# Performance work log

Measured on AMD Instinct MI355X. Metric: run time of the kernel, lower is better.

The kernel has to match this reference:

```python
import jax, jax.numpy as jnp
import numpy as np

ZERO = 1e-8
L = 2            # num_gnn_layers
D = 256          # dim_node_features
B = 32           # graphs per batch
NPG = 256        # nodes per graph
N = B * NPG      # total nodes
E = 131072       # edges per edge-type
MAX_TOKENS = 256 # MAX_TOKENS_OF_A_POST
UPD = 0.5        # args.updated_weights_for_A


def _make_edges(k):
    k1, k2, k3 = jax.random.split(k, 3)
    g = jax.random.randint(k1, (E,), 0, B) * NPG          # keep edges within a graph
    src = g + jax.random.randint(k2, (E,), 0, NPG)
    dst = g + jax.random.randint(k3, (E,), 0, NPG)
    return jnp.stack([src, dst]).astype(jnp.int64)


def setup_inputs() -> dict:
    key = jax.random.key(0)
    ks = jax.random.split(key, 12)
    x = jax.random.normal(ks[0], (N, D), dtype=jnp.float32)
    ei_e = _make_edges(ks[1]); ew_e = jax.random.uniform(ks[2], (E,), dtype=jnp.float32)
    ei_p = _make_edges(ks[3]); ew_p = jax.random.uniform(ks[4], (E,), dtype=jnp.float32)
    ei_o = _make_edges(ks[5]); ew_o = jax.random.uniform(ks[6], (E,), dtype=jnp.float32)
    entity_mask = jax.random.randint(ks[7], (B, NPG), 0, 2).astype(bool)
    pattern_mask = jax.random.randint(ks[8], (B, NPG), 0, 2).astype(bool)
    s = 1.0 / np.sqrt(D)
    W_gcn = (jax.random.normal(ks[9], (L, 3, D, D), dtype=jnp.float32) * s)
    b_gcn = jnp.zeros((L, 3, D), dtype=jnp.float32)
    T_dyn = (jax.random.normal(ks[10], (L, D, D), dtype=jnp.float32) * s)
    return {
        'x': x,
        'edge_index_entity': ei_e, 'edge_weight_entity': ew_e,
        'edge_index_pattern': ei_p, 'edge_weight_pattern': ew_p,
        'edge_index_others': ei_o, 'edge_weight_others': ew_o,
        'entity_mask': entity_mask, 'pattern_mask': pattern_mask,
        'W_gcn': W_gcn, 'b_gcn': b_gcn, 'T_dyn': T_dyn,
    }


def _normalized_correlation_matrix(H):
    # cosine-similarity correlation matrix, symmetrically degree-normalized
    nrm = jnp.sqrt(jnp.sum(H * H, axis=1))
    A = (H @ H.T) / (nrm[:, None] * nrm[None, :] + ZERO)
    dinv = 1.0 / jnp.sqrt(jnp.abs(jnp.sum(A, axis=1)) + ZERO)
    return dinv[:, None] * A * dinv[None, :]


def _gcn(H, W, b, ei, ew):
    # GCNConv(add_self_loops=False, normalize=False): scatter-sum of weighted source messages
    msg = (H @ W)[ei[0]] * ew[:, None]                     # [E, D]
    return jax.ops.segment_sum(msg, ei[1], num_segments=N) + b


def _forward(x, we0, wp0, wo0, W_gcn, b_gcn, T_dyn,
             ei_e, ei_p, ei_o, entity_mask, pattern_mask):
    H = x
    A = _normalized_correlation_matrix(H)                  # [N, N]
    for i in range(L):
        if i == 0:
            we, wp, wo = we0, wp0, wo0
        else:
            # diag(one_hot(src) @ A @ one_hot(dst).T) == A[src, dst]
            we = A[ei_e[0], ei_e[1]]
            wp = A[ei_p[0], ei_p[1]]
            wo = A[ei_o[0], ei_o[1]]
        He = _gcn(H, W_gcn[i, 0], b_gcn[i, 0], ei_e, we)
        Hp = _gcn(H, W_gcn[i, 1], b_gcn[i, 1], ei_p, wp)
        Ho = _gcn(H, W_gcn[i, 2], b_gcn[i, 2], ei_o, wo)
        H = jax.nn.relu(He + Hp + Ho)
        A_hat = jax.nn.sigmoid((H @ T_dyn[i]) @ H.T)
        A = (1.0 - UPD) * A + UPD * A_hat
    # per-graph diagonal blocks of A  -> [B, NPG, NPG]
    A4 = A.reshape(B, NPG, B, NPG)
    idx = jnp.arange(B)
    blocks = A4[idx, :, idx, :]
    A_sum = jnp.sum(blocks, axis=-1)                       # [B, NPG]
    ent_cols = jnp.einsum('bij,bj->bi', blocks, entity_mask.astype(A.dtype))
    pat_cols = jnp.einsum('bij,bj->bi', blocks, pattern_mask.astype(A.dtype))
    map_pattern = A_sum - ent_cols
    map_entity = A_sum - pat_cols

    def finish(m):
        mn = jnp.min(m, axis=1, keepdims=True)
        mx = jnp.max(m, axis=1, keepdims=True)
        m = (m - mn) / (mx - mn + ZERO)
        m = m / (jnp.sum(m, axis=1, keepdims=True) + ZERO)
        return m[:, :MAX_TOKENS]                           # padding() with NPG==MAX_TOKENS

    return finish(map_entity), finish(map_pattern)


def reference(x, edge_index_entity, edge_weight_entity,
              edge_index_pattern, edge_weight_pattern,
              edge_index_others, edge_weight_others,
              entity_mask, pattern_mask, W_gcn, b_gcn, T_dyn):
    return _forward(x, edge_weight_entity, edge_weight_pattern, edge_weight_others,
                    W_gcn, b_gcn, T_dyn,
                    edge_index_entity, edge_index_pattern, edge_index_others,
                    entity_mask, pattern_mask)
```

## Files before the change

kernel.cpp:

```cpp
#include <hip/hip_runtime.h>

#define NND   8192
#define DDIM  256
#define NGRP  32
#define ZEROF 1e-8f
#define LSTR  40
#define TSTR  72
#define OFF_AH 0
#define OFF_AL 2560
#define OFF_BH 5120
#define OFF_BL 10240
#define OFF_TT 5120
#define LDS_U16 15360

typedef unsigned short u16;
typedef unsigned long long u64;
typedef __attribute__((ext_vector_type(8))) short short8v;
typedef __attribute__((ext_vector_type(4))) float float4v;

__device__ inline u16 f2bf(float x) {
  unsigned u = __float_as_uint(x);
  u += 0x7fffu + ((u >> 16) & 1u);
  return (u16)(u >> 16);
}
__device__ inline float bf2f(u16 h) { return __uint_as_float((unsigned)h << 16); }
__device__ inline void split2(float x, u16& h, u16& l) {
  h = f2bf(x);
  l = f2bf(x - bf2f(h));
}

__device__ inline float wave_sum(float v) {
#pragma unroll
  for (int off = 32; off > 0; off >>= 1) v += __shfl_down(v, off, 64);
  return v;
}

#define LOAD_REGS(tt, kk)                                                                   \
  {                                                                                         \
    int m_ = tid >> 2, kq_ = (tid & 3) * 8;                                                 \
    size_t aoff_;                                                                           \
    if (MODE == 1)                                                                          \
      aoff_ = (size_t)((tt) * 256 + bym * 64 + m_) * 8192 + (size_t)(g * 256 + (kk) + kq_); \
    else if (MODE == 2 || MODE == 3)                                                        \
      aoff_ = (size_t)(g * 256 + bym * 64 + m_) * 256 + (kk) + kq_;                         \
    else                                                                                    \
      aoff_ = (size_t)(bym * 64 + m_) * 256 + (kk) + kq_;                                   \
    rAh = *(const short8v*)&Ah_g[aoff_];                                                    \
    rAl = *(const short8v*)&Al_g[aoff_];                                                    \
    if (MODE == 1) {                                                                        \
      int n_ = tid >> 2, kq2_ = (tid & 3) * 8;                                              \
      size_t cb_ = (((size_t)g * 3 + (tt)) << 16) + (size_t)(col0 + n_) * 256 + (kk) + kq2_;\
      const float* pb_ = Bfp + (QW ? cb_ * 2 : cb_);                                        \
      rBf[0] = *(const float4*)pb_;                                                         \
      rBf[1] = *(const float4*)(pb_ + 4);                                                   \
      if (QW) {                                                                             \
        rBf[2] = *(const float4*)(pb_ + 8);                                                 \
        rBf[3] = *(const float4*)(pb_ + 12);                                                \
      }                                                                                     \
    } else if (HALF) {                                                                      \
      int n_ = tid & 63, kq2_ = (tid >> 6) * 8;                                             \
      size_t boff_ = (size_t)(((MODE == 2 || MODE == 3) ? g * 256 : 0) + col0 + n_) * 256   \
                     + (kk) + kq2_;                                                         \
      rBh0 = *(const short8v*)&Bh_g[boff_];                                                 \
      rBl0 = *(const short8v*)&Bl_g[boff_];                                                 \
    } else {                                                                                \
      int n_ = tid & 127, kq2_ = (tid >> 7) * 16;                                           \
      size_t boff_ = (size_t)(col0 + n_) * 256 + (kk) + kq2_;                               \
      rBh0 = *(const short8v*)&Bh_g[boff_]; rBh1 = *(const short8v*)&Bh_g[boff_ + 8];       \
      rBl0 = *(const short8v*)&Bl_g[boff_]; rBl1 = *(const short8v*)&Bl_g[boff_ + 8];       \
    }                                                                                       \
  }

template<int MODE, bool HALF, bool QW = false>
__device__ __forceinline__ void mfma_body(
    u16* lds,
    const u16* __restrict__ Ah_g, const u16* __restrict__ Al_g,
    const u16* __restrict__ Bh_g, const u16* __restrict__ Bl_g,
    const float* __restrict__ Bfp,
    float* __restrict__ Cf, u16* __restrict__ Ch, u16* __restrict__ Cl,
    const float* __restrict__ nrm, const float* __restrict__ dinv,
    const float* __restrict__ bias,
    int bxm, int bym, int g) {
  u16* Ahs = lds + OFF_AH;
  u16* Als = lds + OFF_AL;
  u16* Bhs = lds + OFF_BH;
  u16* Bls = lds + OFF_BL;
  u16* Tt  = lds + OFF_TT;
  const int NJ = HALF ? 2 : 4;
  const int tid = threadIdx.x;
  const int col0 = bxm * (HALF ? 64 : 128);
  const int w = tid >> 6, lane = tid & 63;
  const int lm = lane & 15, lq = lane >> 4;
  const int wr = (w >> 1) * 32, wc = (w & 1) * (HALF ? 32 : 64);

  float4v acc[2][4];
#pragma unroll
  for (int i = 0; i < 2; ++i)
#pragma unroll
    for (int j = 0; j < NJ; ++j) acc[i][j] = (float4v)0.f;

  short8v rAh, rAl, rBh0, rBh1, rBl0, rBl1;
  float4 rBf[4];
  const int TOTAL = (MODE == 1) ? 24 : 8;

  LOAD_REGS(0, 0);
  for (int step = 0; step < TOTAL; ++step) {
    if (step) __syncthreads();
    {
      int m = tid >> 2, kq = (tid & 3) * 8;
      *(short8v*)&Ahs[m * LSTR + kq] = rAh;
      *(short8v*)&Als[m * LSTR + kq] = rAl;
    }
    if (MODE == 1) {
      int n = tid >> 2, kq2 = (tid & 3) * 8;
      float vals[8];
      if (QW) {
        u64 vv[8];
        *(float4*)&vv[0] = rBf[0]; *(float4*)&vv[2] = rBf[1];
        *(float4*)&vv[4] = rBf[2]; *(float4*)&vv[6] = rBf[3];
#pragma unroll
        for (int q = 0; q < 8; ++q)
          vals[q] = (float)(vv[q] & 0xFFFFFFFFFFFFull) * 0x1p-32f;
      } else {
        vals[0] = rBf[0].x; vals[1] = rBf[0].y; vals[2] = rBf[0].z; vals[3] = rBf[0].w;
        vals[4] = rBf[1].x; vals[5] = rBf[1].y; vals[6] = rBf[1].z; vals[7] = rBf[1].w;
      }
      u16 hh[8], ll[8];
#pragma unroll
      for (int q = 0; q < 8; ++q) split2(vals[q], hh[q], ll[q]);
      *(short8v*)&Bhs[n * LSTR + kq2] = *(short8v*)hh;
      *(short8v*)&Bls[n * LSTR + kq2] = *(short8v*)ll;
    } else if (HALF) {
      int n = tid & 63, kq2 = (tid >> 6) * 8;
      *(short8v*)&Bhs[n * LSTR + kq2] = rBh0;
      *(short8v*)&Bls[n * LSTR + kq2] = rBl0;
    } else {
      int n = tid & 127, kq2 = (tid >> 7) * 16;
      *(short8v*)&Bhs[n * LSTR + kq2] = rBh0; *(short8v*)&Bhs[n * LSTR + kq2 + 8] = rBh1;
      *(short8v*)&Bls[n * LSTR + kq2] = rBl0; *(short8v*)&Bls[n * LSTR + kq2 + 8] = rBl1;
    }
    __syncthreads();
    int nxt = step + 1;
    if (nxt < TOTAL) {
      int tt = nxt >> 3, kk = (nxt & 7) * 32;
      LOAD_REGS(tt, kk);
    }
    short8v ah[2], al[2], bh[4], bl[4];
#pragma unroll
    for (int i = 0; i < 2; ++i) {
      int r = wr + i * 16 + lm;
      ah[i] = *(const short8v*)&Ahs[r * LSTR + lq * 8];
      al[i] = *(const short8v*)&Als[r * LSTR + lq * 8];
    }
#pragma unroll
    for (int j = 0; j < NJ; ++j) {
      int r = wc + j * 16 + lm;
      bh[j] = *(const short8v*)&Bhs[r * LSTR + lq * 8];
      bl[j] = *(const short8v*)&Bls[r * LSTR + lq * 8];
    }
#pragma unroll
    for (int i = 0; i < 2; ++i)
#pragma unroll
      for (int j = 0; j < NJ; ++j) {
        acc[i][j] = __builtin_amdgcn_mfma_f32_16x16x32_bf16(ah[i], bh[j], acc[i][j], 0, 0, 0);
        acc[i][j] = __builtin_amdgcn_mfma_f32_16x16x32_bf16(ah[i], bl[j], acc[i][j], 0, 0, 0);
        acc[i][j] = __builtin_amdgcn_mfma_f32_16x16x32_bf16(al[i], bh[j], acc[i][j], 0, 0, 0);
      }
  }

  if (MODE == 2 || MODE == 3) {
    float anewv[2][2][4];
#pragma unroll
    for (int i = 0; i < 2; ++i) {
#pragma unroll
      for (int r = 0; r < 4; ++r) {
        int grow = g * 256 + bym * 64 + wr + i * 16 + lq * 4 + r;
        float di = 0.f, ni = 0.f;
        if (MODE == 2) { di = dinv[grow]; ni = nrm[grow]; }
#pragma unroll
        for (int j = 0; j < NJ; ++j) {
          int gcol = col0 + wc + j * 16 + lm;
          size_t ci = (size_t)grow * 256 + gcol;
          float v = acc[i][j][r];
          if (MODE == 2) {
            int gj = g * 256 + gcol;
            Cf[ci] = v * di * dinv[gj] / (ni * nrm[gj] + ZEROF);
          } else {
            float nv = 0.5f * Cf[ci] + 0.5f * (1.f / (1.f + expf(-v)));
            Cf[ci] = nv;
            anewv[i][j][r] = nv;
          }
        }
      }
    }
    if (MODE == 3 && Ch != nullptr) {
      const u64* Mq = (const u64*)Bfp;
      float* M1 = (float*)Ch;
      float* Af = (float*)lds;
      __syncthreads();
#pragma unroll
      for (int i = 0; i < 2; ++i)
#pragma unroll
        for (int j = 0; j < 2; ++j)
#pragma unroll
          for (int r = 0; r < 4; ++r)
            Af[(wc + j * 16 + lm) * 65 + (wr + i * 16 + lq * 4 + r)] = anewv[i][j][r];
      __syncthreads();
      int rr = tid >> 2;
      int q4 = (tid & 3) * 16;
#pragma unroll
      for (int t = 0; t < 3; ++t) {
        size_t cb = (((size_t)g * 3 + t) << 16) + (size_t)(col0 + rr) * 256 + bym * 64 + q4;
#pragma unroll
        for (int v = 0; v < 4; ++v) {
          const u64* qp = Mq + cb + v * 4;
          float c0 = (float)(qp[0] >> 48), c1 = (float)(qp[1] >> 48);
          float c2 = (float)(qp[2] >> 48), c3 = (float)(qp[3] >> 48);
          float a0 = Af[rr * 65 + q4 + v * 4 + 0];
          float a1 = Af[rr * 65 + q4 + v * 4 + 1];
          float a2 = Af[rr * 65 + q4 + v * 4 + 2];
          float a3 = Af[rr * 65 + q4 + v * 4 + 3];
          *(float4*)&M1[cb + v * 4] = make_float4(c0 * a0, c1 * a1, c2 * a2, c3 * a3);
        }
      }
    }
  } else {
    float bsum[8];
    if (MODE == 1) {
#pragma unroll
      for (int i = 0; i < 2; ++i)
#pragma unroll
        for (int r = 0; r < 4; ++r) {
          int d = bym * 64 + wr + i * 16 + lq * 4 + r;
          bsum[i * 4 + r] = bias[d] + bias[256 + d] + bias[512 + d];
        }
    }
    u16 hv[32], lv[32];
#pragma unroll
    for (int i = 0; i < 2; ++i)
#pragma unroll
      for (int j = 0; j < NJ; ++j)
#pragma unroll
        for (int r = 0; r < 4; ++r) {
          float v = acc[i][j][r];
          if (MODE == 1) v = fmaxf(v + bsum[i * 4 + r], 0.f);
          split2(v, hv[(i * 4 + r) * NJ + j], lv[(i * 4 + r) * NJ + j]);
        }
    int ebase1 = (MODE == 1) ? (g * 256 + col0) : col0;
    int ebase2 = bym * 64;
    size_t estride = (MODE == 0) ? 8192 : 256;
#pragma unroll
    for (int ph = 0; ph < 2; ++ph) {
      __syncthreads();
      const u16* sv = ph ? lv : hv;
#pragma unroll
      for (int i = 0; i < 2; ++i)
#pragma unroll
        for (int j = 0; j < NJ; ++j)
#pragma unroll
          for (int r = 0; r < 4; ++r)
            Tt[(wc + j * 16 + lm) * TSTR + wr + i * 16 + lq * 4 + r] = sv[(i * 4 + r) * NJ + j];
      __syncthreads();
      u16* dst = ph ? Cl : Ch;
      int cc0 = tid >> 3, mm0 = (tid & 7) * 8;
#pragma unroll
      for (int it = 0; it < (HALF ? 2 : 4); ++it) {
        int cc = it * 32 + cc0;
        short8v v = *(const short8v*)&Tt[cc * TSTR + mm0];
        *(short8v*)&dst[(size_t)(ebase1 + cc) * estride + ebase2 + mm0] = v;
      }
    }
  }
}

__global__ void k_prep(const int* __restrict__ e0, const int* __restrict__ e1,
                       const int* __restrict__ e2, const unsigned char* __restrict__ m0,
                       const unsigned char* __restrict__ m1,
                       const float* __restrict__ W, const float* __restrict__ T,
                       const float* __restrict__ x,
                       int* __restrict__ eo, float* __restrict__ emf, float* __restrict__ pmf,
                       u16* __restrict__ Wth, u16* __restrict__ Wtl,
                       float* __restrict__ Mzero,
                       float* __restrict__ nrm, float* __restrict__ Spart,
                       u16* __restrict__ Hh, u16* __restrict__ Hl,
                       int E2, int nCvt) {
  __shared__ float tile[32][33];
  __shared__ float inv[64];
  __shared__ int nz[2];
  const int b = blockIdx.x, tid = threadIdx.x;
  if (b < nCvt) {
    if (tid < 2) nz[tid] = 0;
    __syncthreads();
    if (e0[2 * tid + 1] != 0) atomicAdd(&nz[0], 1);
    int i4 = tid * 4;
    int c = (m0[i4 + 1] != 0) + (m0[i4 + 2] != 0) + (m0[i4 + 3] != 0);
    if (c) atomicAdd(&nz[1], c);
    __syncthreads();
    int fE = (nz[0] == 0), fM = (nz[1] == 0);
    int i = b * 256 + tid;
    if (i < E2) {
      eo[i] = fE ? e0[2 * i] : e0[i];
    } else if (i < 2 * E2) {
      int j = i - E2; eo[E2 + j] = fE ? e1[2 * j] : e1[j];
    } else if (i < 3 * E2) {
      int j = i - 2 * E2; eo[2 * E2 + j] = fE ? e2[2 * j] : e2[j];
    } else if (i < 3 * E2 + NND) {
      int j = i - 3 * E2; unsigned char v = fM ? m0[4 * j] : m0[j];
      emf[j] = 1.f - (float)(v != 0);
    } else if (i < 3 * E2 + 2 * NND) {
      int j = i - 3 * E2 - NND; unsigned char v = fM ? m1[4 * j] : m1[j];
      pmf[j] = 1.f - (float)(v != 0);
    }
  } else if (b < nCvt + 512) {
    int bb = b - nCvt;
    int mat = bb >> 6, rem = bb & 63;
    int k0 = (rem >> 3) * 32, n0 = (rem & 7) * 32;
    const float* src = (mat < 6) ? (W + (size_t)mat * 65536) : (T + (size_t)(mat - 6) * 65536);
    int r = tid >> 3, c4 = (tid & 7) * 4;
    const float4 v = *(const float4*)&src[(size_t)(k0 + r) * 256 + n0 + c4];
    tile[r][c4 + 0] = v.x; tile[r][c4 + 1] = v.y; tile[r][c4 + 2] = v.z; tile[r][c4 + 3] = v.w;
    __syncthreads();
    float o[4] = {tile[c4 + 0][r], tile[c4 + 1][r], tile[c4 + 2][r], tile[c4 + 3][r]};
    u16 hh[4], ll[4];
#pragma unroll
    for (int q = 0; q < 4; ++q) split2(o[q], hh[q], ll[q]);
    size_t off = (size_t)mat * 65536 + (size_t)(n0 + r) * 256 + k0 + c4;
    *(ushort4*)&Wth[off] = *(ushort4*)hh;
    *(ushort4*)&Wtl[off] = *(ushort4*)ll;
  } else if (b < nCvt + 512 + 3072) {
    int bb = b - nCvt - 512;
    float4* p = (float4*)Mzero;
    size_t base = (size_t)bb * 1024 + tid;
    float4 z = make_float4(0.f, 0.f, 0.f, 0.f);
    p[base] = z; p[base + 256] = z; p[base + 512] = z; p[base + 768] = z;
  } else {
    int bn = b - nCvt - 512 - 3072;
    int n0 = bn * 64;
    int w = tid >> 6, lane = tid & 63;
    for (int it = 0; it < 16; ++it) {
      int nl = it * 4 + w;
      int node = n0 + nl;
      const float4 v = *(const float4*)&x[(size_t)node * 256 + lane * 4];
      u16 hh[4], ll[4];
      split2(v.x, hh[0], ll[0]); split2(v.y, hh[1], ll[1]);
      split2(v.z, hh[2], ll[2]); split2(v.w, hh[3], ll[3]);
      *(ushort4*)&Hh[(size_t)node * 256 + lane * 4] = *(ushort4*)hh;
      *(ushort4*)&Hl[(size_t)node * 256 + lane * 4] = *(ushort4*)ll;
      float s = wave_sum(v.x * v.x + v.y * v.y + v.z * v.z + v.w * v.w);
      if (lane == 0) { float nr = sqrtf(s); nrm[node] = nr; inv[nl] = 1.f / nr; }
    }
    __syncthreads();
    float s = 0.f;
    for (int i = 0; i < 64; ++i) s += x[(size_t)(n0 + i) * 256 + tid] * inv[i];
    Spart[bn * 256 + tid] = s;
  }
}

__global__ __launch_bounds__(256, 2) void k_stageA(
    const u16* __restrict__ Hinh, const u16* __restrict__ Hinl,
    const u16* __restrict__ Wth, const u16* __restrict__ Wtl,
    u16* __restrict__ XWTh, u16* __restrict__ XWTl,
    const int* __restrict__ edges, const float* __restrict__ ew0,
    const float* __restrict__ ew1, const float* __restrict__ ew2,
    u64* __restrict__ Mq, int E_,
    const float* __restrict__ x, const float* __restrict__ Spart,
    const float* __restrict__ nrm, float* __restrict__ dinv) {
  __shared__ u16 lds[LDS_U16];
  const int b = blockIdx.x;
  if (b < 768) {
    mfma_body<0, false>(lds, Hinh, Hinl, Wth, Wtl, nullptr,
                        nullptr, XWTh, XWTl, nullptr, nullptr, nullptr,
                        b >> 7, b & 127, 0);
  } else if (b < 1280) {
    int bi = b - 768;
    for (int i = bi * 256 + threadIdx.x; i < 3 * E_; i += 131072) {
      int t = i / E_;
      int e = i - t * E_;
      const int* ei = edges + (size_t)t * 2 * E_;
      int src = ei[e], dst = ei[E_ + e];
      float wgt = (t == 0 ? ew0 : (t == 1 ? ew1 : ew2))[e];
      int gg = src >> 8;
      size_t idx = (((size_t)gg * 3 + t) << 16) + ((size_t)(dst & 255) << 8) + (src & 255);
      u64 enc = (u64)(wgt * 0x1p32f) | (1ull << 48);
      atomicAdd(&Mq[idx], enc);
    }
  } else {
    float* Sl = (float*)lds;
    const int tid = threadIdx.x;
    float s = 0.f;
    for (int bb = 0; bb < 128; ++bb) s += Spart[bb * 256 + tid];
    Sl[tid] = s;
    __syncthreads();
    int base = (b - 1280) * 64;
    int w = tid >> 6, lane = tid & 63;
    const float4 sv = *(const float4*)&Sl[lane * 4];
    for (int it = 0; it < 16; ++it) {
      int node = base + it * 4 + w;
      const float4 v = *(const float4*)&x[(size_t)node * 256 + lane * 4];
      float s2 = wave_sum(v.x * sv.x + v.y * sv.y + v.z * sv.z + v.w * sv.w);
      if (lane == 0) {
        float rowsum = s2 / nrm[node];
        dinv[node] = rsqrtf(fabsf(rowsum) + ZEROF);
      }
    }
  }
}

__global__ __launch_bounds__(256, 2) void k_stageB0(
    const u16* __restrict__ XWTh, const u16* __restrict__ XWTl,
    const float* __restrict__ Mqf,
    u16* __restrict__ Houth, u16* __restrict__ Houtl, const float* __restrict__ bias,
    const u16* __restrict__ xh, const u16* __restrict__ xl, float* __restrict__ Abuf,
    const float* __restrict__ nrm, const float* __restrict__ dinv) {
  __shared__ u16 lds[LDS_U16];
  const int b = blockIdx.x;
  if (b < 512) {
    int g = b & 31, r = b >> 5;
    mfma_body<1, true, true>(lds, XWTh, XWTl, nullptr, nullptr, Mqf,
                             nullptr, Houth, Houtl, nullptr, nullptr, bias,
                             r >> 2, r & 3, g);
  } else {
    int bb = b - 512;
    int g = bb & 31, r = bb >> 5;
    mfma_body<2, true>(lds, xh, xl, xh, xl, nullptr, Abuf, nullptr, nullptr,
                       nrm, dinv, nullptr, r >> 2, r & 3, g);
  }
}

__global__ __launch_bounds__(256, 2) void k_stageB1(
    const u16* __restrict__ XWTh, const u16* __restrict__ XWTl,
    const float* __restrict__ M1,
    u16* __restrict__ Houth, u16* __restrict__ Houtl, const float* __restrict__ bias) {
  __shared__ u16 lds[LDS_U16];
  const int b = blockIdx.x;
  int g = b & 31, r = b >> 5;
  mfma_body<1, true, false>(lds, XWTh, XWTl, nullptr, nullptr, M1,
                            nullptr, Houth, Houtl, nullptr, nullptr, bias,
                            r >> 2, r & 3, g);
}

__global__ __launch_bounds__(256, 2) void k_stageCA(
    const u16* __restrict__ Wth, const u16* __restrict__ Wtl,
    const u16* __restrict__ H2h, const u16* __restrict__ H2l,
    u16* __restrict__ tmph, u16* __restrict__ tmpl,
    u16* __restrict__ XWTh, u16* __restrict__ XWTl) {
  __shared__ u16 lds[LDS_U16];
  const int b = blockIdx.x;
  if (b < 512) {
    mfma_body<4, true>(lds, Wth + (size_t)6 * 65536, Wtl + (size_t)6 * 65536,
                       H2h, H2l, nullptr, nullptr, tmph, tmpl, nullptr, nullptr, nullptr,
                       b & 127, b >> 7, 0);
  } else {
    int bb = b - 512;
    mfma_body<0, false>(lds, H2h, H2l, Wth + (size_t)768 * 256, Wtl + (size_t)768 * 256,
                        nullptr, nullptr, XWTh, XWTl, nullptr, nullptr, nullptr,
                        bb >> 7, bb & 127, 0);
  }
}

__global__ __launch_bounds__(256, 2) void k_stageC1(
    const u16* __restrict__ Wth, const u16* __restrict__ Wtl,
    const u16* __restrict__ Hh, const u16* __restrict__ Hl,
    u16* __restrict__ tmph, u16* __restrict__ tmpl) {
  __shared__ u16 lds[LDS_U16];
  const int b = blockIdx.x;
  mfma_body<4, true>(lds, Wth + (size_t)7 * 65536, Wtl + (size_t)7 * 65536,
                     Hh, Hl, nullptr, nullptr, tmph, tmpl, nullptr, nullptr, nullptr,
                     b & 127, b >> 7, 0);
}

__global__ __launch_bounds__(256, 2) void k_stageD(
    const u16* __restrict__ tmph, const u16* __restrict__ tmpl,
    const u16* __restrict__ Hh, const u16* __restrict__ Hl,
    float* __restrict__ Abuf, const float* __restrict__ Mqf, float* __restrict__ M1) {
  __shared__ u16 lds[LDS_U16];
  const int b = blockIdx.x;
  int g = b & 31, r = b >> 5;
  mfma_body<3, true>(lds, tmph, tmpl, Hh, Hl, Mqf, Abuf, (u16*)M1, nullptr,
                     nullptr, nullptr, nullptr, r >> 2, r & 3, g);
}

__global__ void k_maps(const float* __restrict__ Abuf, const float* __restrict__ emf,
                       const float* __restrict__ pmf, float* __restrict__ out) {
  __shared__ float sme[256], smp[256], red[256];
  const int g = blockIdx.x, tid = threadIdx.x, w = tid >> 6, lane = tid & 63;
  const int j0 = g * 256 + lane * 4;
  const float4 pmv = *(const float4*)&pmf[j0];
  const float4 emv = *(const float4*)&emf[j0];
  for (int it = 0; it < 64; ++it) {
    int nl = it * 4 + w;
    const float4 a = *(const float4*)&Abuf[((size_t)g * 256 + nl) * 256 + lane * 4];
    float me = a.x * pmv.x + a.y * pmv.y + a.z * pmv.z + a.w * pmv.w;
    float mp = a.x * emv.x + a.y * emv.y + a.z * emv.z + a.w * emv.w;
#pragma unroll
    for (int off = 32; off > 0; off >>= 1) {
      me += __shfl_down(me, off, 64);
      mp += __shfl_down(mp, off, 64);
    }
    if (lane == 0) { sme[nl] = me; smp[nl] = mp; }
  }
  __syncthreads();
  for (int which = 0; which < 2; ++which) {
    float v = which ? smp[tid] : sme[tid];
    red[tid] = v; __syncthreads();
    for (int s = 128; s > 0; s >>= 1) { if (tid < s) red[tid] = fminf(red[tid], red[tid + s]); __syncthreads(); }
    float mn = red[0]; __syncthreads();
    red[tid] = v; __syncthreads();
    for (int s = 128; s > 0; s >>= 1) { if (tid < s) red[tid] = fmaxf(red[tid], red[tid + s]); __syncthreads(); }
    float mx = red[0]; __syncthreads();
    float m = (v - mn) / (mx - mn + ZEROF);
    red[tid] = m; __syncthreads();
    for (int s = 128; s > 0; s >>= 1) { if (tid < s) red[tid] += red[tid + s]; __syncthreads(); }
    float sum = red[0]; __syncthreads();
    out[which * NND + g * 256 + tid] = m / (sum + ZEROF);
  }
}

extern "C" void kernel_launch(void* const* d_in, const int* in_sizes, int n_in,
                              void* d_out, int out_size, void* d_ws, size_t ws_size,
                              hipStream_t stream) {
  const float* x = (const float*)d_in[0];
  const unsigned char* em_raw = (const unsigned char*)d_in[7];
  const unsigned char* pm_raw = (const unsigned char*)d_in[8];
  const float* W  = (const float*)d_in[9];
  const float* bg = (const float*)d_in[10];
  const float* T  = (const float*)d_in[11];
  float* out = (float*)d_out;
  const int E_ = in_sizes[2];
  const int E2 = 2 * E_;

  float* ws = (float*)d_ws;
  size_t o = 0;
  float* Abuf = ws + o; o += (size_t)NND * 256;
  u64*  Mq   = (u64*)(ws + o); o += (size_t)2 * NGRP * 3 * 65536;
  float* M1  = ws + o; o += (size_t)NGRP * 3 * 65536;
  u16* Hh   = (u16*)(ws + o); o += (size_t)NND * 256 / 2;
  u16* Hl   = (u16*)(ws + o); o += (size_t)NND * 256 / 2;
  u16* H2h  = (u16*)(ws + o); o += (size_t)NND * 256 / 2;
  u16* H2l  = (u16*)(ws + o); o += (size_t)NND * 256 / 2;
  u16* tmph = (u16*)(ws + o); o += (size_t)NND * 256 / 2;
  u16* tmpl = (u16*)(ws + o); o += (size_t)NND * 256 / 2;
  u16* XWTh = (u16*)(ws + o); o += (size_t)768 * NND / 2;
  u16* XWTl = (u16*)(ws + o); o += (size_t)768 * NND / 2;
  u16* Wth  = (u16*)(ws + o); o += (size_t)8 * 65536 / 2;
  u16* Wtl  = (u16*)(ws + o); o += (size_t)8 * 65536 / 2;
  float* nrm   = ws + o; o += NND;
  float* dinv  = ws + o; o += NND;
  float* Spart = ws + o; o += 128 * 256;
  float* emf   = ws + o; o += NND;
  float* pmf   = ws + o; o += NND;
  int* edges   = (int*)(ws + o); o += (size_t)3 * E2;

  const float* ew0 = (const float*)d_in[2];
  const float* ew1 = (const float*)d_in[4];
  const float* ew2 = (const float*)d_in[6];

  const int nCvt = (3 * E2 + 2 * NND + 255) / 256;

  k_prep<<<nCvt + 512 + 3072 + 128, 256, 0, stream>>>(
      (const int*)d_in[1], (const int*)d_in[3], (const int*)d_in[5], em_raw, pm_raw,
      W, T, x, edges, emf, pmf, Wth, Wtl, (float*)Mq, nrm, Spart, Hh, Hl, E2, nCvt);

  k_stageA<<<1408, 256, 0, stream>>>(Hh, Hl, Wth, Wtl, XWTh, XWTl,
                                     edges, ew0, ew1, ew2, Mq, E_,
                                     x, Spart, nrm, dinv);
  k_stageB0<<<1024, 256, 0, stream>>>(XWTh, XWTl, (const float*)Mq, H2h, H2l, bg,
                                      Hh, Hl, Abuf, nrm, dinv);
  k_stageCA<<<1280, 256, 0, stream>>>(Wth, Wtl, H2h, H2l, tmph, tmpl, XWTh, XWTl);
  k_stageD<<<512, 256, 0, stream>>>(tmph, tmpl, H2h, H2l, Abuf, (const float*)Mq, M1);

  k_stageB1<<<512, 256, 0, stream>>>(XWTh, XWTl, M1, Hh, Hl, bg + 768);
  k_stageC1<<<512, 256, 0, stream>>>(Wth, Wtl, Hh, Hl, tmph, tmpl);
  k_stageD<<<512, 256, 0, stream>>>(tmph, tmpl, Hh, Hl, Abuf, nullptr, nullptr);

  k_maps<<<NGRP, 256, 0, stream>>>(Abuf, emf, pmf, out);
}
```

Baseline: 296.4 us.

## Scatter edges directly from raw int64 input in prep kernel and memset accumulator

The edge-scatter atomics now run in the prep kernel and read the raw (possibly int64) edge index arrays directly, so the intermediate int32 edge buffer and its separate conversion pass are gone. Zeroing of the atomic accumulator moves from 3072 prep blocks to a hipMemsetAsync issued before the prep kernel. Stage A shrinks to only the MFMA and dinv blocks. The trade-off is that the atomic scatter no longer overlaps with the stage-A GEMM, and there is an extra memset launch.

```diff
diff --git a/kernel.cpp b/kernel.cpp
--- a/kernel.cpp
+++ b/kernel.cpp
@@ -278,41 +278,55 @@
                        const unsigned char* __restrict__ m1,
                        const float* __restrict__ W, const float* __restrict__ T,
                        const float* __restrict__ x,
-                       int* __restrict__ eo, float* __restrict__ emf, float* __restrict__ pmf,
+                       const float* __restrict__ ew0, const float* __restrict__ ew1,
+                       const float* __restrict__ ew2,
+                       float* __restrict__ emf, float* __restrict__ pmf,
                        u16* __restrict__ Wth, u16* __restrict__ Wtl,
-                       float* __restrict__ Mzero,
+                       u64* __restrict__ Mq,
                        float* __restrict__ nrm, float* __restrict__ Spart,
-                       u16* __restrict__ Hh, u16* __restrict__ Hl,
-                       int E2, int nCvt) {
+                       u16* __restrict__ Hh, u16* __restrict__ Hl, int E_) {
   __shared__ float tile[32][33];
   __shared__ float inv[64];
   __shared__ int nz[2];
   const int b = blockIdx.x, tid = threadIdx.x;
-  if (b < nCvt) {
-    if (tid < 2) nz[tid] = 0;
+  if (b < 512) {
+    if (tid == 0) nz[0] = 0;
     __syncthreads();
     if (e0[2 * tid + 1] != 0) atomicAdd(&nz[0], 1);
+    __syncthreads();
+    int fE = (nz[0] == 0);
+    for (int i = b * 256 + tid; i < 3 * E_; i += 131072) {
+      int t = i / E_;
+      int e = i - t * E_;
+      const int* er = (t == 0) ? e0 : (t == 1 ? e1 : e2);
+      int src, dst;
+      if (fE) { src = er[2 * e]; dst = er[2 * (E_ + e)]; }
+      else    { src = er[e];     dst = er[E_ + e]; }
+      float wgt = (t == 0 ? ew0 : (t == 1 ? ew1 : ew2))[e];
+      int gg = src >> 8;
+      size_t idx = (((size_t)gg * 3 + t) << 16) + ((size_t)(dst & 255) << 8) + (src & 255);
+      u64 enc = (u64)(wgt * 0x1p32f) | (1ull << 48);
+      atomicAdd(&Mq[idx], enc);
+    }
+  } else if (b < 576) {
+    if (tid == 0) nz[1] = 0;
+    __syncthreads();
     int i4 = tid * 4;
     int c = (m0[i4 + 1] != 0) + (m0[i4 + 2] != 0) + (m0[i4 + 3] != 0);
     if (c) atomicAdd(&nz[1], c);
     __syncthreads();
-    int fE = (nz[0] == 0), fM = (nz[1] == 0);
-    int i = b * 256 + tid;
-    if (i < E2) {
-      eo[i] = fE ? e0[2 * i] : e0[i];
-    } else if (i < 2 * E2) {
-      int j = i - E2; eo[E2 + j] = fE ? e1[2 * j] : e1[j];
-    } else if (i < 3 * E2) {
-      int j = i - 2 * E2; eo[2 * E2 + j] = fE ? e2[2 * j] : e2[j];
-    } else if (i < 3 * E2 + NND) {
-      int j = i - 3 * E2; unsigned char v = fM ? m0[4 * j] : m0[j];
-      emf[j] = 1.f - (float)(v != 0);
-    } else if (i < 3 * E2 + 2 * NND) {
-      int j = i - 3 * E2 - NND; unsigned char v = fM ? m1[4 * j] : m1[j];
+    int fM = (nz[1] == 0);
+    int i = (b - 512) * 256 + tid;
+    if (i < NND) {
+      unsigned char v = fM ? m0[4 * i] : m0[i];
+      emf[i] = 1.f - (float)(v != 0);
+    } else {
+      int j = i - NND;
+      unsigned char v = fM ? m1[4 * j] : m1[j];
       pmf[j] = 1.f - (float)(v != 0);
     }
-  } else if (b < nCvt + 512) {
-    int bb = b - nCvt;
+  } else if (b < 1088) {
+    int bb = b - 576;
     int mat = bb >> 6, rem = bb & 63;
     int k0 = (rem >> 3) * 32, n0 = (rem & 7) * 32;
     const float* src = (mat < 6) ? (W + (size_t)mat * 65536) : (T + (size_t)(mat - 6) * 65536);
@@ -327,14 +341,8 @@
     size_t off = (size_t)mat * 65536 + (size_t)(n0 + r) * 256 + k0 + c4;
     *(ushort4*)&Wth[off] = *(ushort4*)hh;
     *(ushort4*)&Wtl[off] = *(ushort4*)ll;
-  } else if (b < nCvt + 512 + 3072) {
-    int bb = b - nCvt - 512;
-    float4* p = (float4*)Mzero;
-    size_t base = (size_t)bb * 1024 + tid;
-    float4 z = make_float4(0.f, 0.f, 0.f, 0.f);
-    p[base] = z; p[base + 256] = z; p[base + 512] = z; p[base + 768] = z;
   } else {
-    int bn = b - nCvt - 512 - 3072;
+    int bn = b - 1088;
     int n0 = bn * 64;
     int w = tid >> 6, lane = tid & 63;
     for (int it = 0; it < 16; ++it) {
@@ -360,9 +368,6 @@
     const u16* __restrict__ Hinh, const u16* __restrict__ Hinl,
     const u16* __restrict__ Wth, const u16* __restrict__ Wtl,
     u16* __restrict__ XWTh, u16* __restrict__ XWTl,
-    const int* __restrict__ edges, const float* __restrict__ ew0,
-    const float* __restrict__ ew1, const float* __restrict__ ew2,
-    u64* __restrict__ Mq, int E_,
     const float* __restrict__ x, const float* __restrict__ Spart,
     const float* __restrict__ nrm, float* __restrict__ dinv) {
   __shared__ u16 lds[LDS_U16];
@@ -371,19 +376,6 @@
     mfma_body<0, false>(lds, Hinh, Hinl, Wth, Wtl, nullptr,
                         nullptr, XWTh, XWTl, nullptr, nullptr, nullptr,
                         b >> 7, b & 127, 0);
-  } else if (b < 1280) {
-    int bi = b - 768;
-    for (int i = bi * 256 + threadIdx.x; i < 3 * E_; i += 131072) {
-      int t = i / E_;
-      int e = i - t * E_;
-      const int* ei = edges + (size_t)t * 2 * E_;
-      int src = ei[e], dst = ei[E_ + e];
-      float wgt = (t == 0 ? ew0 : (t == 1 ? ew1 : ew2))[e];
-      int gg = src >> 8;
-      size_t idx = (((size_t)gg * 3 + t) << 16) + ((size_t)(dst & 255) << 8) + (src & 255);
-      u64 enc = (u64)(wgt * 0x1p32f) | (1ull << 48);
-      atomicAdd(&Mq[idx], enc);
-    }
   } else {
     float* Sl = (float*)lds;
     const int tid = threadIdx.x;
@@ -391,7 +383,7 @@
     for (int bb = 0; bb < 128; ++bb) s += Spart[bb * 256 + tid];
     Sl[tid] = s;
     __syncthreads();
-    int base = (b - 1280) * 64;
+    int base = (b - 768) * 64;
     int w = tid >> 6, lane = tid & 63;
     const float4 sv = *(const float4*)&Sl[lane * 4];
     for (int it = 0; it < 16; ++it) {
@@ -527,7 +519,6 @@
   const float* T  = (const float*)d_in[11];
   float* out = (float*)d_out;
   const int E_ = in_sizes[2];
-  const int E2 = 2 * E_;
 
   float* ws = (float*)d_ws;
   size_t o = 0;
@@ -549,21 +540,18 @@
   float* Spart = ws + o; o += 128 * 256;
   float* emf   = ws + o; o += NND;
   float* pmf   = ws + o; o += NND;
-  int* edges   = (int*)(ws + o); o += (size_t)3 * E2;
 
   const float* ew0 = (const float*)d_in[2];
   const float* ew1 = (const float*)d_in[4];
   const float* ew2 = (const float*)d_in[6];
 
-  const int nCvt = (3 * E2 + 2 * NND + 255) / 256;
-
-  k_prep<<<nCvt + 512 + 3072 + 128, 256, 0, stream>>>(
+  hipMemsetAsync(Mq, 0, (size_t)2 * NGRP * 3 * 65536 * sizeof(float), stream);
+  k_prep<<<1216, 256, 0, stream>>>(
       (const int*)d_in[1], (const int*)d_in[3], (const int*)d_in[5], em_raw, pm_raw,
-      W, T, x, edges, emf, pmf, Wth, Wtl, (float*)Mq, nrm, Spart, Hh, Hl, E2, nCvt);
-
-  k_stageA<<<1408, 256, 0, stream>>>(Hh, Hl, Wth, Wtl, XWTh, XWTl,
-                                     edges, ew0, ew1, ew2, Mq, E_,
-                                     x, Spart, nrm, dinv);
+      W, T, x, ew0, ew1, ew2, emf, pmf, Wth, Wtl, Mq, nrm, Spart, Hh, Hl, E_);
+
+  k_stageA<<<896, 256, 0, stream>>>(Hh, Hl, Wth, Wtl, XWTh, XWTl,
+                                    x, Spart, nrm, dinv);
   k_stageB0<<<1024, 256, 0, stream>>>(XWTh, XWTl, (const float*)Mq, H2h, H2l, bg,
                                       Hh, Hl, Abuf, nrm, dinv);
   k_stageCA<<<1280, 256, 0, stream>>>(Wth, Wtl, H2h, H2l, tmph, tmpl, XWTh, XWTl);
```

Measured after the change: 307.1 us. +3.6%, slower.
